# Performance work log

Measured on AMD Instinct MI355X. Metric: run time of the kernel, lower is better.

## Reference

```python
import jax, jax.numpy as jnp
import numpy as np

ALPHA = 0.2
NEG = -9e15
EPS = 1e-5


def _gat(h, adj, W, a, out_features):
    # h: [B,N,Fin], adj: [B,N,N], W: [Fin,Fout], a: [2*Fout,1]
    Wh = jnp.matmul(h, W)                      # [B,N,Fout]
    Wh1 = jnp.matmul(Wh, a[:out_features])     # [B,N,1]
    Wh2 = jnp.matmul(Wh, a[out_features:])     # [B,N,1]
    e = Wh1 + jnp.swapaxes(Wh2, 1, 2)          # [B,N,N]
    e = jax.nn.leaky_relu(e, negative_slope=ALPHA)
    scores = jnp.where(adj > 0, e, NEG)
    att = jax.nn.softmax(scores, axis=1)       # NOTE: dim=1 as in source
    return jnp.matmul(att, Wh)                 # [B,N,Fout]


def _layernorm(x, g, b):
    mu = jnp.mean(x, axis=-1, keepdims=True)
    var = jnp.var(x, axis=-1, keepdims=True)
    return (x - mu) * jax.lax.rsqrt(var + EPS) * g + b


def setup_inputs() -> dict:
    key = jax.random.key(0)
    ks = jax.random.split(key, 8)
    B, N, F, H = 2, 4096, 256, 1024
    x = jax.random.normal(ks[0], (B, N, F), dtype=jnp.float32)
    adj = jax.random.randint(ks[1], (B, N, N), 0, 2, dtype=jnp.int32)
    def xavier(k, shape):
        fan_in, fan_out = shape[0], shape[1]
        lim = np.sqrt(6.0 / (fan_in + fan_out))
        return jax.random.uniform(k, shape, jnp.float32, -lim, lim)
    return {
        "x": x,
        "adj": adj,
        "W1": xavier(ks[2], (F, F)),
        "a1": xavier(ks[3], (2 * F, 1)),
        "W2": xavier(ks[4], (F, F)),
        "a2": xavier(ks[5], (2 * F, 1)),
        "w_ff1": xavier(ks[6], (F, H)) ,
        "b_ff1": jnp.zeros((H,), jnp.float32),
        "w_ff2": xavier(ks[7], (H, F)),
        "b_ff2": jnp.zeros((F,), jnp.float32),
        "g_ln1": jnp.ones((F,), jnp.float32),
        "b_ln1": jnp.zeros((F,), jnp.float32),
        "g_ln2": jnp.ones((F,), jnp.float32),
        "b_ln2": jnp.zeros((F,), jnp.float32),
    }


def reference(x, adj, W1, a1, W2, a2, w_ff1, b_ff1, w_ff2, b_ff2,
              g_ln1, b_ln1, g_ln2, b_ln2):
    Fout = W1.shape[1]
    residual = x
    # dropout is a no-op in eval mode
    h = _gat(x, adj, W1, a1, Fout)          # single head -> cat is identity
    h = _gat(h, adj, W2, a2, W2.shape[1])
    h = _layernorm(residual + h, g_ln1, b_ln1)
    residual2 = h
    ff = jnp.matmul(jax.nn.relu(jnp.matmul(h, w_ff1) + b_ff1), w_ff2) + b_ff2
    return _layernorm(residual2 + ff, g_ln2, b_ln2)
```

## Files before the change

kernel.cpp:

```cpp
#include <hip/hip_runtime.h>
#include <math.h>

#define ALPHA 0.2f
#define NEGV  -9e15f
#define EPSV  1e-5f

constexpr int B_ = 2, N_ = 4096, F_ = 256, H_ = 1024;
constexpr int SPLIT_ = 16;

typedef __attribute__((ext_vector_type(4))) float f32x4;
typedef __attribute__((ext_vector_type(8))) short s16x8;

__device__ __forceinline__ unsigned short f2bf(float f) {
    unsigned u = __builtin_bit_cast(unsigned, f);
    u += 0x7fffu + ((u >> 16) & 1u);
    return (unsigned short)(u >> 16);
}

__global__ __launch_bounds__(256) void zero_kernel(float* __restrict__ p)
{
    const int i = (blockIdx.x * 256 + threadIdx.x) * 4;
    *(float4*)&p[i] = make_float4(0.f, 0.f, 0.f, 0.f);
}

__global__ __launch_bounds__(256) void transp_all_kernel(
    const float* __restrict__ W1, const float* __restrict__ W2,
    const float* __restrict__ F1s, const float* __restrict__ F2s,
    unsigned short* __restrict__ D1, unsigned short* __restrict__ D2,
    unsigned short* __restrict__ D3, unsigned short* __restrict__ D4)
{
    const int mi = blockIdx.z;
    const float* src; unsigned short* dst; int R, Cc;
    if (mi == 0)      { src = W1;  dst = D1; R = 256;  Cc = 256; }
    else if (mi == 1) { src = W2;  dst = D2; R = 256;  Cc = 256; }
    else if (mi == 2) { src = F1s; dst = D3; R = 256;  Cc = 1024; }
    else              { src = F2s; dst = D4; R = 1024; Cc = 256; }
    const int r0 = blockIdx.x * 64, c0 = blockIdx.y * 64;
    if (r0 >= R || c0 >= Cc) return;

    __shared__ float T[64][65];
    const int t = threadIdx.x;
    #pragma unroll
    for (int s = 0; s < 4; ++s) {
        const int rr = s * 16 + (t >> 4);
        const int cq = t & 15;
        const float4 v = *(const float4*)&src[(size_t)(r0 + rr) * Cc + c0 + cq * 4];
        T[rr][cq * 4 + 0] = v.x; T[rr][cq * 4 + 1] = v.y;
        T[rr][cq * 4 + 2] = v.z; T[rr][cq * 4 + 3] = v.w;
    }
    __syncthreads();
    #pragma unroll
    for (int s = 0; s < 4; ++s) {
        const int cr = s * 16 + (t >> 4);
        const int rq = t & 15;
        ushort4 o;
        o.x = f2bf(T[rq * 4 + 0][cr]);
        o.y = f2bf(T[rq * 4 + 1][cr]);
        o.z = f2bf(T[rq * 4 + 2][cr]);
        o.w = f2bf(T[rq * 4 + 3][cr]);
        *(ushort4*)&dst[(size_t)(c0 + cr) * R + r0 + rq * 4] = o;
    }
}

__global__ __launch_bounds__(256) void gemm128_kernel(
    const void* __restrict__ Ap, const unsigned short* __restrict__ Wt,
    const float* __restrict__ bias, void* __restrict__ Cp,
    unsigned short* __restrict__ Tout, const float* __restrict__ wha,
    float* __restrict__ Wh1, float* __restrict__ Wh2,
    int Nc, int K, int relu, int a_bf16, int c_mode)
{
    __shared__ unsigned short As[128 * 72];
    __shared__ unsigned short Bs[128 * 72];
    const int t = threadIdx.x;
    const int w = t >> 6, l = t & 63;
    const int quad = l >> 4, l15 = l & 15;
    const int wr = w & 1, wc = w >> 1;
    const int row0 = blockIdx.y * 128, col0 = blockIdx.x * 128;
    const int sr = t >> 1;
    const int sk = (t & 1) * 32;

    f32x4 acc[4][4];
    #pragma unroll
    for (int it = 0; it < 4; ++it)
        #pragma unroll
        for (int ft = 0; ft < 4; ++ft) acc[it][ft] = (f32x4)(0.f);

    for (int k0 = 0; k0 < K; k0 += 64) {
        if (a_bf16) {
            const unsigned short* ap =
                (const unsigned short*)Ap + (size_t)(row0 + sr) * K + k0 + sk;
            #pragma unroll
            for (int u = 0; u < 4; ++u)
                *(s16x8*)&As[sr * 72 + sk + u * 8] = *(const s16x8*)(ap + u * 8);
        } else {
            const float* ap = (const float*)Ap + (size_t)(row0 + sr) * K + k0 + sk;
            #pragma unroll
            for (int u = 0; u < 8; ++u) {
                const float4 v = *(const float4*)(ap + u * 4);
                ushort4 o;
                o.x = f2bf(v.x); o.y = f2bf(v.y); o.z = f2bf(v.z); o.w = f2bf(v.w);
                *(ushort4*)&As[sr * 72 + sk + u * 4] = o;
            }
        }
        {
            const unsigned short* bp = Wt + (size_t)(col0 + sr) * K + k0 + sk;
            #pragma unroll
            for (int u = 0; u < 4; ++u)
                *(s16x8*)&Bs[sr * 72 + sk + u * 8] = *(const s16x8*)(bp + u * 8);
        }
        __syncthreads();
        #pragma unroll
        for (int ks = 0; ks < 64; ks += 32) {
            s16x8 af[4], bf[4];
            #pragma unroll
            for (int it = 0; it < 4; ++it)
                af[it] = *(const s16x8*)&As[(wr * 64 + it * 16 + l15) * 72 + ks + quad * 8];
            #pragma unroll
            for (int ft = 0; ft < 4; ++ft)
                bf[ft] = *(const s16x8*)&Bs[(wc * 64 + ft * 16 + l15) * 72 + ks + quad * 8];
            #pragma unroll
            for (int ft = 0; ft < 4; ++ft)
                #pragma unroll
                for (int it = 0; it < 4; ++it)
                    acc[it][ft] = __builtin_amdgcn_mfma_f32_16x16x32_bf16(
                        af[it], bf[ft], acc[it][ft], 0, 0, 0);
        }
        __syncthreads();
    }

    if (c_mode) {
        #pragma unroll
        for (int ft = 0; ft < 4; ++ft) {
            const int col = col0 + wc * 64 + ft * 16 + l15;
            const float bv = bias ? bias[col] : 0.f;
            #pragma unroll
            for (int it = 0; it < 4; ++it) {
                const int rbase = row0 + wr * 64 + it * 16 + quad * 4;
                #pragma unroll
                for (int rr = 0; rr < 4; ++rr) {
                    float v = acc[it][ft][rr] + bv;
                    if (relu) v = fmaxf(v, 0.f);
                    if (c_mode == 2)
                        ((unsigned short*)Cp)[(size_t)(rbase + rr) * Nc + col] = f2bf(v);
                    else
                        ((float*)Cp)[(size_t)(rbase + rr) * Nc + col] = v;
                }
            }
        }
    }

    if (Tout) {
        const int bb = row0 >> 12;
        #pragma unroll
        for (int ft = 0; ft < 4; ++ft) {
            const int col = col0 + wc * 64 + ft * 16 + l15;
            #pragma unroll
            for (int it = 0; it < 4; ++it) {
                const int ibase = (row0 & (N_ - 1)) + wr * 64 + it * 16 + quad * 4;
                ushort4 o;
                o.x = f2bf(acc[it][ft][0]); o.y = f2bf(acc[it][ft][1]);
                o.z = f2bf(acc[it][ft][2]); o.w = f2bf(acc[it][ft][3]);
                *(ushort4*)&Tout[((size_t)bb * F_ + col) * N_ + ibase] = o;
            }
        }
    }

    if (wha) {
        float a1v[4], a2v[4];
        #pragma unroll
        for (int ft = 0; ft < 4; ++ft) {
            const int col = col0 + wc * 64 + ft * 16 + l15;
            a1v[ft] = wha[col];
            a2v[ft] = wha[F_ + col];
        }
        #pragma unroll
        for (int it = 0; it < 4; ++it)
            #pragma unroll
            for (int rr = 0; rr < 4; ++rr) {
                float s1 = 0.f, s2 = 0.f;
                #pragma unroll
                for (int ft = 0; ft < 4; ++ft) {
                    s1 += acc[it][ft][rr] * a1v[ft];
                    s2 += acc[it][ft][rr] * a2v[ft];
                }
                #pragma unroll
                for (int mkk = 1; mkk < 16; mkk <<= 1) {
                    s1 += __shfl_xor(s1, mkk);
                    s2 += __shfl_xor(s2, mkk);
                }
                if (l15 == 0) {
                    const int row = row0 + wr * 64 + it * 16 + quad * 4 + rr;
                    atomicAdd(&Wh1[row], s1);
                    atomicAdd(&Wh2[row], s2);
                }
            }
    }
}

__global__ __launch_bounds__(256) void gemm64_kernel(
    const void* __restrict__ Ap, const unsigned short* __restrict__ Wt,
    const float* __restrict__ bias, void* __restrict__ Cp,
    unsigned short* __restrict__ Tout, const float* __restrict__ wha,
    float* __restrict__ Wh1, float* __restrict__ Wh2,
    int Nc, int K, int relu, int a_bf16, int c_mode)
{
    __shared__ unsigned short As[64 * 72];
    __shared__ unsigned short Bs[128 * 72];
    const int t = threadIdx.x;
    const int w = t >> 6, l = t & 63;
    const int quad = l >> 4, l15 = l & 15;
    const int row0 = blockIdx.y * 64, col0 = blockIdx.x * 128;
    const int sra = t >> 2;
    const int ska = (t & 3) * 16;
    const int srb = t >> 1;
    const int skb = (t & 1) * 32;

    f32x4 acc[4][2];
    #pragma unroll
    for (int it = 0; it < 4; ++it)
        #pragma unroll
        for (int ft = 0; ft < 2; ++ft) acc[it][ft] = (f32x4)(0.f);

    for (int k0 = 0; k0 < K; k0 += 64) {
        if (a_bf16) {
            const unsigned short* ap =
                (const unsigned short*)Ap + (size_t)(row0 + sra) * K + k0 + ska;
            *(s16x8*)&As[sra * 72 + ska]     = *(const s16x8*)ap;
            *(s16x8*)&As[sra * 72 + ska + 8] = *(const s16x8*)(ap + 8);
        } else {
            const float* ap = (const float*)Ap + (size_t)(row0 + sra) * K + k0 + ska;
            #pragma unroll
            for (int u = 0; u < 4; ++u) {
                const float4 v = *(const float4*)(ap + u * 4);
                ushort4 o;
                o.x = f2bf(v.x); o.y = f2bf(v.y); o.z = f2bf(v.z); o.w = f2bf(v.w);
                *(ushort4*)&As[sra * 72 + ska + u * 4] = o;
            }
        }
        {
            const unsigned short* bp = Wt + (size_t)(col0 + srb) * K + k0 + skb;
            #pragma unroll
            for (int u = 0; u < 4; ++u)
                *(s16x8*)&Bs[srb * 72 + skb + u * 8] = *(const s16x8*)(bp + u * 8);
        }
        __syncthreads();
        #pragma unroll
        for (int ks = 0; ks < 64; ks += 32) {
            s16x8 af[4], bf[2];
            #pragma unroll
            for (int it = 0; it < 4; ++it)
                af[it] = *(const s16x8*)&As[(it * 16 + l15) * 72 + ks + quad * 8];
            #pragma unroll
            for (int ft = 0; ft < 2; ++ft)
                bf[ft] = *(const s16x8*)&Bs[(w * 32 + ft * 16 + l15) * 72 + ks + quad * 8];
            #pragma unroll
            for (int ft = 0; ft < 2; ++ft)
                #pragma unroll
                for (int it = 0; it < 4; ++it)
                    acc[it][ft] = __builtin_amdgcn_mfma_f32_16x16x32_bf16(
                        af[it], bf[ft], acc[it][ft], 0, 0, 0);
        }
        __syncthreads();
    }

    if (c_mode) {
        #pragma unroll
        for (int ft = 0; ft < 2; ++ft) {
            const int col = col0 + w * 32 + ft * 16 + l15;
            const float bv = bias ? bias[col] : 0.f;
            #pragma unroll
            for (int it = 0; it < 4; ++it) {
                const int rbase = row0 + it * 16 + quad * 4;
                #pragma unroll
                for (int rr = 0; rr < 4; ++rr) {
                    float v = acc[it][ft][rr] + bv;
                    if (relu) v = fmaxf(v, 0.f);
                    if (c_mode == 2)
                        ((unsigned short*)Cp)[(size_t)(rbase + rr) * Nc + col] = f2bf(v);
                    else
                        ((float*)Cp)[(size_t)(rbase + rr) * Nc + col] = v;
                }
            }
        }
    }

    if (Tout) {
        const int bb = row0 >> 12;
        #pragma unroll
        for (int ft = 0; ft < 2; ++ft) {
            const int col = col0 + w * 32 + ft * 16 + l15;
            #pragma unroll
            for (int it = 0; it < 4; ++it) {
                const int ibase = (row0 & (N_ - 1)) + it * 16 + quad * 4;
                ushort4 o;
                o.x = f2bf(acc[it][ft][0]); o.y = f2bf(acc[it][ft][1]);
                o.z = f2bf(acc[it][ft][2]); o.w = f2bf(acc[it][ft][3]);
                *(ushort4*)&Tout[((size_t)bb * F_ + col) * N_ + ibase] = o;
            }
        }
    }

    if (wha) {
        float a1v[2], a2v[2];
        #pragma unroll
        for (int ft = 0; ft < 2; ++ft) {
            const int col = col0 + w * 32 + ft * 16 + l15;
            a1v[ft] = wha[col];
            a2v[ft] = wha[F_ + col];
        }
        #pragma unroll
        for (int it = 0; it < 4; ++it)
            #pragma unroll
            for (int rr = 0; rr < 4; ++rr) {
                float s1 = acc[it][0][rr] * a1v[0] + acc[it][1][rr] * a1v[1];
                float s2 = acc[it][0][rr] * a2v[0] + acc[it][1][rr] * a2v[1];
                #pragma unroll
                for (int mkk = 1; mkk < 16; mkk <<= 1) {
                    s1 += __shfl_xor(s1, mkk);
                    s2 += __shfl_xor(s2, mkk);
                }
                if (l15 == 0) {
                    const int row = row0 + it * 16 + quad * 4 + rr;
                    atomicAdd(&Wh1[row], s1);
                    atomicAdd(&Wh2[row], s2);
                }
            }
    }
}

__global__ __launch_bounds__(256) void colstats_adj_kernel(
    const int* __restrict__ adj, unsigned long long* __restrict__ maskOut,
    const float* __restrict__ Wh1, const float* __restrict__ Wh2,
    float* __restrict__ pM, float* __restrict__ pS)
{
    const int t = threadIdx.x;
    const int j = blockIdx.x * 256 + t;
    const int sp = blockIdx.y;
    const int b = blockIdx.z;
    const int i0 = sp * (N_ / SPLIT_);
    const int w = t >> 6, l = t & 63;
    const float w2 = Wh2[b * N_ + j];
    const float* __restrict__ w1p = Wh1 + b * N_ + i0;
    const int* __restrict__ ap = adj + ((size_t)b * N_ + i0) * N_ + j;

    float m = -3.4e38f, s = 0.f;
    for (int c = 0; c < N_ / SPLIT_; c += 8) {
        int v[8];
        #pragma unroll
        for (int u = 0; u < 8; ++u) v[u] = ap[(size_t)(c + u) * N_];
        float x[8];
        #pragma unroll
        for (int u = 0; u < 8; ++u) {
            const bool act = v[u] > 0;
            const unsigned long long bm = __ballot(act);
            if (l == 0)
                maskOut[((size_t)b * N_ + i0 + c + u) * (N_ / 64) + blockIdx.x * 4 + w] = bm;
            const float e0 = w1p[c + u] + w2;
            const float e = fmaxf(e0, ALPHA * e0);
            x[u] = act ? e : NEGV;
        }
        const float cm = fmaxf(fmaxf(fmaxf(x[0], x[1]), fmaxf(x[2], x[3])),
                               fmaxf(fmaxf(x[4], x[5]), fmaxf(x[6], x[7])));
        const float nm = fmaxf(m, cm);
        float cs = 0.f;
        #pragma unroll
        for (int u = 0; u < 8; ++u) cs += __expf(x[u] - nm);
        s = s * __expf(m - nm) + cs;
        m = nm;
    }
    pM[((size_t)b * SPLIT_ + sp) * N_ + j] = m;
    pS[((size_t)b * SPLIT_ + sp) * N_ + j] = s;
}

__global__ __launch_bounds__(256) void colstats3_kernel(
    const unsigned long long* __restrict__ mask,
    const float* __restrict__ Wh1, const float* __restrict__ Wh2,
    float* __restrict__ pM, float* __restrict__ pS)
{
    const int t = threadIdx.x;
    const int j = blockIdx.x * 256 + t;
    const int sp = blockIdx.y;
    const int b = blockIdx.z;
    const int i0 = sp * (N_ / SPLIT_);
    const int w = t >> 6;
    const int jbit = t & 63;
    const float w2 = Wh2[b * N_ + j];
    const unsigned long long* __restrict__ mbase =
        mask + ((size_t)b * N_ + i0) * (N_ / 64) + blockIdx.x * 4 + w;
    const float* __restrict__ w1p = Wh1 + b * N_ + i0;

    float m = -3.4e38f, s = 0.f;
    for (int c = 0; c < N_ / SPLIT_; c += 8) {
        float x[8];
        #pragma unroll
        for (int u = 0; u < 8; ++u) {
            const unsigned long long mw = mbase[(size_t)(c + u) * (N_ / 64)];
            const float e0 = w1p[c + u] + w2;
            const float e = fmaxf(e0, ALPHA * e0);
            x[u] = ((mw >> jbit) & 1ull) ? e : NEGV;
        }
        const float cm = fmaxf(fmaxf(fmaxf(x[0], x[1]), fmaxf(x[2], x[3])),
                               fmaxf(fmaxf(x[4], x[5]), fmaxf(x[6], x[7])));
        const float nm = fmaxf(m, cm);
        float cs = 0.f;
        #pragma unroll
        for (int u = 0; u < 8; ++u) cs += __expf(x[u] - nm);
        s = s * __expf(m - nm) + cs;
        m = nm;
    }
    pM[((size_t)b * SPLIT_ + sp) * N_ + j] = m;
    pS[((size_t)b * SPLIT_ + sp) * N_ + j] = s;
}

__global__ __launch_bounds__(256) void colfin2_kernel(
    const float* __restrict__ pM, const float* __restrict__ pS,
    float* __restrict__ Mo)
{
    const int j = blockIdx.x * 256 + threadIdx.x;
    const int b = blockIdx.y;
    float m = -3.4e38f;
    #pragma unroll
    for (int s = 0; s < SPLIT_; ++s)
        m = fmaxf(m, pM[((size_t)b * SPLIT_ + s) * N_ + j]);
    float sum = 0.f;
    #pragma unroll
    for (int s = 0; s < SPLIT_; ++s)
        sum += pS[((size_t)b * SPLIT_ + s) * N_ + j] *
               __expf(pM[((size_t)b * SPLIT_ + s) * N_ + j] - m);
    Mo[b * N_ + j] = m + logf(sum);
}

__global__ __launch_bounds__(512) void att_mfma5_kernel(
    const unsigned short* __restrict__ mask16, const unsigned short* __restrict__ Wht,
    const float* __restrict__ Wh1, const float* __restrict__ Wh2,
    const float* __restrict__ Mo, unsigned short* __restrict__ outb,
    float* __restrict__ outf)
{
    __shared__ unsigned short Ps[2][32 * 72];
    __shared__ float w2s[N_];
    __shared__ float mos[N_];

    const int t = threadIdx.x;
    const int w = t >> 6, l = t & 63;
    const int quad = l >> 4, l15 = l & 15;

    const int lin = blockIdx.x;
    const int xcd = lin & 7;
    const int b = xcd >> 2;
    const int tile = (lin >> 3) * 4 + (xcd & 3);
    const int i0 = tile * 32;

    const int pi = t >> 4;
    const int pj = t & 15;
    const float w1i = Wh1[b * N_ + i0 + pi];
    const unsigned short* __restrict__ mrow =
        mask16 + ((size_t)b * N_ + i0 + pi) * (N_ / 16);
    const unsigned short* __restrict__ WhtB = Wht + (size_t)b * F_ * N_;

    {
        const float4 a0 = *(const float4*)&Wh2[b * N_ + t * 8];
        const float4 a1 = *(const float4*)&Wh2[b * N_ + t * 8 + 4];
        const float4 c0 = *(const float4*)&Mo[b * N_ + t * 8];
        const float4 c1 = *(const float4*)&Mo[b * N_ + t * 8 + 4];
        *(float4*)&w2s[t * 8] = a0; *(float4*)&w2s[t * 8 + 4] = a1;
        *(float4*)&mos[t * 8] = c0; *(float4*)&mos[t * 8 + 4] = c1;
    }

    f32x4 acc[2][2];
    #pragma unroll
    for (int it = 0; it < 2; ++it)
        #pragma unroll
        for (int ft = 0; ft < 2; ++ft) acc[it][ft] = (f32x4)(0.f);

    const unsigned short* __restrict__ bbase =
        WhtB + (size_t)(w * 32 + l15) * N_ + quad * 8;

    s16x8 bA[4], bB[4];

    auto prefB = [&](int itr2, s16x8* dst) {
        const unsigned short* nb = bbase + itr2 * 64;
        #pragma unroll
        for (int ft = 0; ft < 2; ++ft)
            #pragma unroll
            for (int kk = 0; kk < 2; ++kk)
                dst[ft * 2 + kk] = *(const s16x8*)&nb[(size_t)ft * 16 * N_ + kk * 32];
    };

    auto computeP = [&](int itr2, unsigned short* psdst) {
        const unsigned mb = mrow[itr2 * 4 + (pj >> 2)];
        const int bsh = (pj & 3) * 4;
        const int jl = itr2 * 64 + pj * 4;
        const float4 w2v = *(const float4*)&w2s[jl];
        const float4 mov = *(const float4*)&mos[jl];
        ushort4 o;
        unsigned short* op = &o.x;
        #pragma unroll
        for (int u = 0; u < 4; ++u) {
            const float xw = w1i + (&w2v.x)[u];
            const float e = fmaxf(xw, ALPHA * xw);
            const float x2 = ((mb >> (bsh + u)) & 1u) ? e : NEGV;
            op[u] = f2bf(__expf(x2 - (&mov.x)[u]));
        }
        *(ushort4*)&psdst[pi * 72 + pj * 4] = o;
    };

    auto mfmaStep = [&](const unsigned short* ps, const s16x8* breg) {
        #pragma unroll
        for (int ksidx = 0; ksidx < 2; ++ksidx) {
            s16x8 af[2];
            #pragma unroll
            for (int it = 0; it < 2; ++it)
                af[it] = *(const s16x8*)&ps[(it * 16 + l15) * 72 + ksidx * 32 + quad * 8];
            #pragma unroll
            for (int ft = 0; ft < 2; ++ft)
                #pragma unroll
                for (int it = 0; it < 2; ++it)
                    acc[it][ft] = __builtin_amdgcn_mfma_f32_16x16x32_bf16(
                        af[it], breg[ft * 2 + ksidx], acc[it][ft], 0, 0, 0);
        }
    };

    prefB(0, bA);
    __syncthreads();
    computeP(0, &Ps[0][0]);
    __syncthreads();

    constexpr int NITER = N_ / 64;
    for (int itr = 0; itr < NITER; itr += 2) {
        prefB(itr + 1, bB);
        computeP(itr + 1, &Ps[1][0]);
        mfmaStep(&Ps[0][0], bA);
        __syncthreads();
        if (itr + 2 < NITER) {
            prefB(itr + 2, bA);
            computeP(itr + 2, &Ps[0][0]);
        }
        mfmaStep(&Ps[1][0], bB);
        __syncthreads();
    }

    if (outb) {
        unsigned short* __restrict__ ob = outb + (size_t)(b * N_ + i0) * F_;
        #pragma unroll
        for (int it = 0; it < 2; ++it)
            #pragma unroll
            for (int ft = 0; ft < 2; ++ft) {
                const int col = w * 32 + ft * 16 + l15;
                #pragma unroll
                for (int rr = 0; rr < 4; ++rr)
                    ob[(size_t)(it * 16 + quad * 4 + rr) * F_ + col] =
                        f2bf(acc[it][ft][rr]);
            }
    } else {
        float* __restrict__ of = outf + (size_t)(b * N_ + i0) * F_;
        #pragma unroll
        for (int it = 0; it < 2; ++it)
            #pragma unroll
            for (int ft = 0; ft < 2; ++ft) {
                const int col = w * 32 + ft * 16 + l15;
                #pragma unroll
                for (int rr = 0; rr < 4; ++rr)
                    of[(size_t)(it * 16 + quad * 4 + rr) * F_ + col] =
                        acc[it][ft][rr];
            }
    }
}

__global__ __launch_bounds__(256) void addln2b_kernel(
    const float* __restrict__ X, const float* __restrict__ Y,
    const float* __restrict__ g, const float* __restrict__ bta,
    float* __restrict__ outf, unsigned short* __restrict__ outb)
{
    const int row = blockIdx.x;
    const int t = threadIdx.x;
    const size_t idx = (size_t)row * F_ + t;
    const float v = X[idx] + Y[idx];
    float s1 = v, s2 = v * v;
    #pragma unroll
    for (int off = 32; off > 0; off >>= 1) {
        s1 += __shfl_down(s1, off);
        s2 += __shfl_down(s2, off);
    }
    __shared__ float r1[4], r2[4];
    __shared__ float mu_s, rs_s;
    const int wid = t >> 6, lane = t & 63;
    if (lane == 0) { r1[wid] = s1; r2[wid] = s2; }
    __syncthreads();
    if (t == 0) {
        const float a = r1[0] + r1[1] + r1[2] + r1[3];
        const float q = r2[0] + r2[1] + r2[2] + r2[3];
        const float mu = a * (1.f / F_);
        const float var = q * (1.f / F_) - mu * mu;
        mu_s = mu;
        rs_s = rsqrtf(var + EPSV);
    }
    __syncthreads();
    const float r = (v - mu_s) * rs_s * g[t] + bta[t];
    outf[idx] = r;
    outb[idx] = f2bf(r);
}

__global__ __launch_bounds__(256) void addln_kernel(
    const float* __restrict__ X, const float* __restrict__ Y,
    const float* __restrict__ g, const float* __restrict__ bta,
    float* __restrict__ out)
{
    const int row = blockIdx.x;
    const int t = threadIdx.x;
    const size_t idx = (size_t)row * F_ + t;
    const float v = X[idx] + Y[idx];
    float s1 = v, s2 = v * v;
    #pragma unroll
    for (int off = 32; off > 0; off >>= 1) {
        s1 += __shfl_down(s1, off);
        s2 += __shfl_down(s2, off);
    }
    __shared__ float r1[4], r2[4];
    __shared__ float mu_s, rs_s;
    const int wid = t >> 6, lane = t & 63;
    if (lane == 0) { r1[wid] = s1; r2[wid] = s2; }
    __syncthreads();
    if (t == 0) {
        const float a = r1[0] + r1[1] + r1[2] + r1[3];
        const float q = r2[0] + r2[1] + r2[2] + r2[3];
        const float mu = a * (1.f / F_);
        const float var = q * (1.f / F_) - mu * mu;
        mu_s = mu;
        rs_s = rsqrtf(var + EPSV);
    }
    __syncthreads();
    out[idx] = (v - mu_s) * rs_s * g[t] + bta[t];
}

extern "C" void kernel_launch(void* const* d_in, const int* in_sizes, int n_in,
                              void* d_out, int out_size, void* d_ws, size_t ws_size,
                              hipStream_t stream)
{
    const float* x     = (const float*)d_in[0];
    const int*   adj   = (const int*)d_in[1];
    const float* W1    = (const float*)d_in[2];
    const float* a1    = (const float*)d_in[3];
    const float* W2    = (const float*)d_in[4];
    const float* a2    = (const float*)d_in[5];
    const float* w_ff1 = (const float*)d_in[6];
    const float* b_ff1 = (const float*)d_in[7];
    const float* w_ff2 = (const float*)d_in[8];
    const float* b_ff2 = (const float*)d_in[9];
    const float* g_ln1 = (const float*)d_in[10];
    const float* b_ln1 = (const float*)d_in[11];
    const float* g_ln2 = (const float*)d_in[12];
    const float* b_ln2 = (const float*)d_in[13];
    float* out = (float*)d_out;

    const int Rtot = B_ * N_;
    char* wsb = (char*)d_ws;
    float* attout = (float*)wsb;
    float* ln1   = (float*)(wsb + 33554432);
    float* ffout = (float*)(wsb + 41943040);
    unsigned short* mid  = (unsigned short*)(wsb + 50331648);
    unsigned short* ln1b = (unsigned short*)(wsb + 67108864);
    unsigned short* g1b  = (unsigned short*)(wsb + 71303168);
    unsigned short* Wht  = (unsigned short*)(wsb + 75497472);
    unsigned long long* mask = (unsigned long long*)(wsb + 79691776);
    unsigned short* mask16 = (unsigned short*)mask;
    unsigned short* Wt1  = (unsigned short*)(wsb + 83886080);
    unsigned short* Wt2  = Wt1 + 65536;
    unsigned short* Wtf1 = Wt2 + 65536;
    unsigned short* Wtf2 = Wtf1 + 262144;
    float* WhA1 = (float*)(wsb + 85196800);
    float* WhA2 = WhA1 + 8192;
    float* WhB1 = WhA2 + 8192;
    float* WhB2 = WhB1 + 8192;
    float* Mo   = (float*)(wsb + 85327872);
    float* pM   = (float*)(wsb + 85360640);
    float* pS   = (float*)(wsb + 85884928);

    const dim3 statsG(N_ / 256, SPLIT_, B_);
    const dim3 finG(N_ / 256, B_);

    zero_kernel<<<32, 256, 0, stream>>>(WhA1);
    transp_all_kernel<<<dim3(16, 16, 4), 256, 0, stream>>>(
        W1, W2, w_ff1, w_ff2, Wt1, Wt2, Wtf1, Wtf2);

    gemm64_kernel<<<dim3(2, 128), 256, 0, stream>>>(
        x, Wt1, nullptr, nullptr, Wht, a1, WhA1, WhA2, F_, F_, 0, 0, 0);
    colstats_adj_kernel<<<statsG, 256, 0, stream>>>(adj, mask, WhA1, WhA2, pM, pS);
    colfin2_kernel<<<finG, 256, 0, stream>>>(pM, pS, Mo);
    att_mfma5_kernel<<<256, 512, 0, stream>>>(
        mask16, Wht, WhA1, WhA2, Mo, g1b, nullptr);

    gemm64_kernel<<<dim3(2, 128), 256, 0, stream>>>(
        g1b, Wt2, nullptr, nullptr, Wht, a2, WhB1, WhB2, F_, F_, 0, 1, 0);
    colstats3_kernel<<<statsG, 256, 0, stream>>>(mask, WhB1, WhB2, pM, pS);
    colfin2_kernel<<<finG, 256, 0, stream>>>(pM, pS, Mo);
    att_mfma5_kernel<<<256, 512, 0, stream>>>(
        mask16, Wht, WhB1, WhB2, Mo, nullptr, attout);

    addln2b_kernel<<<Rtot, 256, 0, stream>>>(x, attout, g_ln1, b_ln1, ln1, ln1b);

    gemm128_kernel<<<dim3(8, 64), 256, 0, stream>>>(
        ln1b, Wtf1, b_ff1, mid, nullptr, nullptr, nullptr, nullptr, H_, F_, 1, 1, 2);
    gemm64_kernel<<<dim3(2, 128), 256, 0, stream>>>(
        mid, Wtf2, b_ff2, ffout, nullptr, nullptr, nullptr, nullptr, F_, H_, 0, 1, 1);

    addln_kernel<<<Rtot, 256, 0, stream>>>(ln1, ffout, g_ln2, b_ln2, out);
}
```

Baseline: 485.1 us.

## Split attention output columns across two blocks and stage mask rows in LDS

The attention-aggregation kernel now splits the 256 output features into two halves, each handled by its own block, which doubles the grid to 512 blocks so the GPU has more parallel work and each block holds fewer accumulators. Each block also preloads its 32 rows of the packed adjacency mask into shared memory up front instead of reading the mask from global memory on every iteration. In exchange, the P-matrix exponentials (mask, leaky-relu, exp) are now computed twice, once per column half. Per-block shared memory also grows by about 17 KB.

```diff
diff --git a/kernel.cpp b/kernel.cpp
--- a/kernel.cpp
+++ b/kernel.cpp
@@ -430,7 +430,7 @@
     Mo[b * N_ + j] = m + logf(sum);
 }
 
-__global__ __launch_bounds__(512) void att_mfma5_kernel(
+__global__ __launch_bounds__(512) void att_mfma6_kernel(
     const unsigned short* __restrict__ mask16, const unsigned short* __restrict__ Wht,
     const float* __restrict__ Wh1, const float* __restrict__ Wh2,
     const float* __restrict__ Mo, unsigned short* __restrict__ outb,
@@ -439,6 +439,7 @@
     __shared__ unsigned short Ps[2][32 * 72];
     __shared__ float w2s[N_];
     __shared__ float mos[N_];
+    __shared__ unsigned short msk[32 * 264];
 
     const int t = threadIdx.x;
     const int w = t >> 6, l = t & 63;
@@ -447,49 +448,35 @@
     const int lin = blockIdx.x;
     const int xcd = lin & 7;
     const int b = xcd >> 2;
-    const int tile = (lin >> 3) * 4 + (xcd & 3);
+    const int half = (xcd >> 1) & 1;
+    const int tile = (lin >> 3) * 2 + (xcd & 1);
     const int i0 = tile * 32;
+    const int c0 = half * 128;
 
     const int pi = t >> 4;
-    const int pj = t & 15;
+    const int pj4 = t & 15;
     const float w1i = Wh1[b * N_ + i0 + pi];
-    const unsigned short* __restrict__ mrow =
-        mask16 + ((size_t)b * N_ + i0 + pi) * (N_ / 16);
     const unsigned short* __restrict__ WhtB = Wht + (size_t)b * F_ * N_;
 
-    {
-        const float4 a0 = *(const float4*)&Wh2[b * N_ + t * 8];
-        const float4 a1 = *(const float4*)&Wh2[b * N_ + t * 8 + 4];
-        const float4 c0 = *(const float4*)&Mo[b * N_ + t * 8];
-        const float4 c1 = *(const float4*)&Mo[b * N_ + t * 8 + 4];
-        *(float4*)&w2s[t * 8] = a0; *(float4*)&w2s[t * 8 + 4] = a1;
-        *(float4*)&mos[t * 8] = c0; *(float4*)&mos[t * 8 + 4] = c1;
-    }
-
-    f32x4 acc[2][2];
-    #pragma unroll
-    for (int it = 0; it < 2; ++it)
-        #pragma unroll
-        for (int ft = 0; ft < 2; ++ft) acc[it][ft] = (f32x4)(0.f);
+    f32x4 acc[2];
+    acc[0] = (f32x4)(0.f);
+    acc[1] = (f32x4)(0.f);
 
     const unsigned short* __restrict__ bbase =
-        WhtB + (size_t)(w * 32 + l15) * N_ + quad * 8;
-
-    s16x8 bA[4], bB[4];
+        WhtB + (size_t)(c0 + w * 16 + l15) * N_ + quad * 8;
+
+    s16x8 bA[2], bB[2];
 
     auto prefB = [&](int itr2, s16x8* dst) {
         const unsigned short* nb = bbase + itr2 * 64;
-        #pragma unroll
-        for (int ft = 0; ft < 2; ++ft)
-            #pragma unroll
-            for (int kk = 0; kk < 2; ++kk)
-                dst[ft * 2 + kk] = *(const s16x8*)&nb[(size_t)ft * 16 * N_ + kk * 32];
+        dst[0] = *(const s16x8*)&nb[0];
+        dst[1] = *(const s16x8*)&nb[32];
     };
 
     auto computeP = [&](int itr2, unsigned short* psdst) {
-        const unsigned mb = mrow[itr2 * 4 + (pj >> 2)];
-        const int bsh = (pj & 3) * 4;
-        const int jl = itr2 * 64 + pj * 4;
+        const unsigned mb = msk[pi * 264 + itr2 * 4 + (pj4 >> 2)];
+        const int bsh = (pj4 & 3) * 4;
+        const int jl = itr2 * 64 + pj4 * 4;
         const float4 w2v = *(const float4*)&w2s[jl];
         const float4 mov = *(const float4*)&mos[jl];
         ushort4 o;
@@ -501,26 +488,32 @@
             const float x2 = ((mb >> (bsh + u)) & 1u) ? e : NEGV;
             op[u] = f2bf(__expf(x2 - (&mov.x)[u]));
         }
-        *(ushort4*)&psdst[pi * 72 + pj * 4] = o;
+        *(ushort4*)&psdst[pi * 72 + pj4 * 4] = o;
     };
 
     auto mfmaStep = [&](const unsigned short* ps, const s16x8* breg) {
         #pragma unroll
-        for (int ksidx = 0; ksidx < 2; ++ksidx) {
-            s16x8 af[2];
-            #pragma unroll
-            for (int it = 0; it < 2; ++it)
-                af[it] = *(const s16x8*)&ps[(it * 16 + l15) * 72 + ksidx * 32 + quad * 8];
-            #pragma unroll
-            for (int ft = 0; ft < 2; ++ft)
-                #pragma unroll
-                for (int it = 0; it < 2; ++it)
-                    acc[it][ft] = __builtin_amdgcn_mfma_f32_16x16x32_bf16(
-                        af[it], breg[ft * 2 + ksidx], acc[it][ft], 0, 0, 0);
+        for (int ks = 0; ks < 2; ++ks) {
+            #pragma unroll
+            for (int it = 0; it < 2; ++it) {
+                const s16x8 af =
+                    *(const s16x8*)&ps[(it * 16 + l15) * 72 + ks * 32 + quad * 8];
+                acc[it] = __builtin_amdgcn_mfma_f32_16x16x32_bf16(
+                    af, breg[ks], acc[it], 0, 0, 0);
+            }
         }
     };
 
     prefB(0, bA);
+    #pragma unroll
+    for (int k2 = 0; k2 < 2; ++k2) {
+        const int i4 = t + k2 * 512;
+        *(float4*)&w2s[i4 * 4] = *(const float4*)&Wh2[b * N_ + i4 * 4];
+        *(float4*)&mos[i4 * 4] = *(const float4*)&Mo[b * N_ + i4 * 4];
+        const int mr = i4 >> 5, mc = i4 & 31;
+        *(s16x8*)&msk[mr * 264 + mc * 8] =
+            *(const s16x8*)&mask16[(size_t)(b * N_ + i0 + mr) * 256 + mc * 8];
+    }
     __syncthreads();
     computeP(0, &Ps[0][0]);
     __syncthreads();
@@ -539,30 +532,21 @@
         __syncthreads();
     }
 
+    const int col = c0 + w * 16 + l15;
     if (outb) {
-        unsigned short* __restrict__ ob = outb + (size_t)(b * N_ + i0) * F_;
+        unsigned short* __restrict__ ob = outb + (size_t)(b * N_ + i0) * F_ + col;
         #pragma unroll
         for (int it = 0; it < 2; ++it)
             #pragma unroll
-            for (int ft = 0; ft < 2; ++ft) {
-                const int col = w * 32 + ft * 16 + l15;
-                #pragma unroll
-                for (int rr = 0; rr < 4; ++rr)
-                    ob[(size_t)(it * 16 + quad * 4 + rr) * F_ + col] =
-                        f2bf(acc[it][ft][rr]);
-            }
+            for (int rr = 0; rr < 4; ++rr)
+                ob[(size_t)(it * 16 + quad * 4 + rr) * F_] = f2bf(acc[it][rr]);
     } else {
-        float* __restrict__ of = outf + (size_t)(b * N_ + i0) * F_;
+        float* __restrict__ of = outf + (size_t)(b * N_ + i0) * F_ + col;
         #pragma unroll
         for (int it = 0; it < 2; ++it)
             #pragma unroll
-            for (int ft = 0; ft < 2; ++ft) {
-                const int col = w * 32 + ft * 16 + l15;
-                #pragma unroll
-                for (int rr = 0; rr < 4; ++rr)
-                    of[(size_t)(it * 16 + quad * 4 + rr) * F_ + col] =
-                        acc[it][ft][rr];
-            }
+            for (int rr = 0; rr < 4; ++rr)
+                of[(size_t)(it * 16 + quad * 4 + rr) * F_] = acc[it][rr];
     }
 }
 
@@ -686,14 +670,14 @@
         x, Wt1, nullptr, nullptr, Wht, a1, WhA1, WhA2, F_, F_, 0, 0, 0);
     colstats_adj_kernel<<<statsG, 256, 0, stream>>>(adj, mask, WhA1, WhA2, pM, pS);
     colfin2_kernel<<<finG, 256, 0, stream>>>(pM, pS, Mo);
-    att_mfma5_kernel<<<256, 512, 0, stream>>>(
+    att_mfma6_kernel<<<512, 512, 0, stream>>>(
         mask16, Wht, WhA1, WhA2, Mo, g1b, nullptr);
 
     gemm64_kernel<<<dim3(2, 128), 256, 0, stream>>>(
         g1b, Wt2, nullptr, nullptr, Wht, a2, WhB1, WhB2, F_, F_, 0, 1, 0);
     colstats3_kernel<<<statsG, 256, 0, stream>>>(mask, WhB1, WhB2, pM, pS);
     colfin2_kernel<<<finG, 256, 0, stream>>>(pM, pS, Mo);
-    att_mfma5_kernel<<<256, 512, 0, stream>>>(
+    att_mfma6_kernel<<<512, 512, 0, stream>>>(
         mask16, Wht, WhB1, WhB2, Mo, nullptr, attout);
 
     addln2b_kernel<<<Rtot, 256, 0, stream>>>(x, attout, g_ln1, b_ln1, ln1, ln1b);
```

After: 452.3 us. 1.07x faster.
